# Kernel optimization log

Measured on AMD Instinct MI355X. Metric: run time of the kernel, lower is better.

Reference implementation:

```python
import jax, jax.numpy as jnp
import numpy as np

T, B, E, H, V = 512, 64, 512, 1024, 256


def setup_inputs() -> dict:
    key = jax.random.key(0)
    ks = jax.random.split(key, 10)
    s = lambda k, shape, sc: jax.random.normal(k, shape, dtype=jnp.float32) * sc
    return {
        "ints": jax.random.randint(ks[0], (T, B), 0, V),
        "encodings": s(ks[1], (V, E), 1.0),
        "output0": s(ks[2], (H,), 1.0),
        "memory0": s(ks[3], (H,), 1.0),
        "W_ih": s(ks[4], (4 * H, E), 0.03),
        "W_hh": s(ks[5], (4 * H, H), 0.03),
        "b_ih": s(ks[6], (4 * H,), 0.03),
        "b_hh": s(ks[7], (4 * H,), 0.03),
        "W_dec": s(ks[8], (V, H), 0.03),
        "b_dec": jnp.zeros((V,), dtype=jnp.float32),
    }


def reference(ints, encodings, output0, memory0, W_ih, W_hh, b_ih, b_hh, W_dec, b_dec):
    t, b = ints.shape
    h = output0.shape[0]
    x = encodings[ints]                                   # [T,B,E] embedding gather
    h0 = jnp.broadcast_to(output0, (b, h))                # learned initial hidden
    c0 = jnp.broadcast_to(memory0, (b, h))                # learned initial cell
    # precompute input projection for all timesteps (one big GEMM)
    x_proj = jnp.einsum('tbe,ge->tbg', x, W_ih) + b_ih + b_hh  # [T,B,4H]

    def step(carry, xp):
        hh, cc = carry
        gates = xp + hh @ W_hh.T                          # [B,4H]
        i, f, g, o = jnp.split(gates, 4, axis=-1)         # torch gate order i,f,g,o
        i = jax.nn.sigmoid(i)
        f = jax.nn.sigmoid(f)
        g = jnp.tanh(g)
        o = jax.nn.sigmoid(o)
        cc = f * cc + i * g
        hh = o * jnp.tanh(cc)
        return (hh, cc), hh

    _, hs = jax.lax.scan(step, (h0, c0), x_proj)          # [T,B,H]
    # outputs shifted right by one: predict char t from state after chars <t
    outs = jnp.concatenate([h0[None], hs[:-1]], axis=0)   # [T,B,H]
    return outs @ W_dec.T + b_dec                          # [T,B,V]
```

## Files before the change

### kernel.cpp

```cpp
#include <hip/hip_runtime.h>


#define TT 512
#define BB 64
#define HH 1024
#define VV 256
#define EE 512

typedef __attribute__((ext_vector_type(8))) short bf16x8;
typedef __attribute__((ext_vector_type(4))) float f32x4;
typedef __attribute__((ext_vector_type(4))) int i32x4;
typedef __attribute__((ext_vector_type(4))) unsigned short u16x4;

static __device__ __forceinline__ unsigned short f2bf(float f) {
  union { float f; unsigned u; } x; x.f = f;
  unsigned r = x.u + 0x7fffu + ((x.u >> 16) & 1u);
  return (unsigned short)(r >> 16);
}

__global__ void cvt_bf16(const float* __restrict__ s, unsigned short* __restrict__ d, int n4) {
  int i = blockIdx.x * blockDim.x + threadIdx.x;
  int st = gridDim.x * blockDim.x;
  for (; i < n4; i += st) {
    f32x4 v = *(const f32x4*)(s + 4l * i);
    u16x4 o;
    o.x = f2bf(v.x); o.y = f2bf(v.y); o.z = f2bf(v.z); o.w = f2bf(v.w);
    *(u16x4*)(d + 4l * i) = o;
  }
}

__global__ __launch_bounds__(256) void proj_kernel(
    const unsigned short* __restrict__ A,
    const unsigned short* __restrict__ Wi,
    const float* __restrict__ bih, const float* __restrict__ bhh,
    float* __restrict__ proj)
{
  __shared__ __align__(16) unsigned char Asm[64 * 128];
  const int tid = threadIdx.x;
  const int w = tid >> 6;
  const int lane = tid & 63;
  const int ln = lane & 15, kg = lane >> 4;
  const int m0 = blockIdx.x * 64;
  const int nb = blockIdx.y * 256 + w * 64;
  const int srow = tid >> 2, skq = tid & 3;

  f32x4 acc[4][4];
  for (int a = 0; a < 4; ++a) for (int b = 0; b < 4; ++b) acc[a][b] = (f32x4){0.f,0.f,0.f,0.f};

  for (int kc = 0; kc < 8; ++kc) {
    {
      const unsigned short* src = A + (m0 + srow) * 512 + kc * 64 + skq * 16;
      unsigned base = (unsigned)(srow * 128 + skq * 32);
      unsigned sw = (unsigned)((srow & 7) << 4);
      *(i32x4*)(Asm + ((base) ^ sw))      = *(const i32x4*)(src);
      *(i32x4*)(Asm + ((base + 16) ^ sw)) = *(const i32x4*)(src + 8);
    }
    __syncthreads();
    for (int kk = 0; kk < 2; ++kk) {
      bf16x8 afr[4];
      for (int mi = 0; mi < 4; ++mi) {
        int row = mi * 16 + ln;
        unsigned off = (unsigned)(row * 128 + (kk * 32 + kg * 8) * 2);
        afr[mi] = *(const bf16x8*)(Asm + (off ^ ((unsigned)(row & 7) << 4)));
      }
      for (int ni = 0; ni < 4; ++ni) {
        const unsigned short* bp = Wi + (nb + ni * 16 + ln) * 512 + kc * 64 + kk * 32 + kg * 8;
        bf16x8 bfr = *(const bf16x8*)bp;
        for (int mi = 0; mi < 4; ++mi)
          acc[mi][ni] = __builtin_amdgcn_mfma_f32_16x16x32_bf16(afr[mi], bfr, acc[mi][ni], 0, 0, 0);
      }
    }
    __syncthreads();
  }
  for (int ni = 0; ni < 4; ++ni) {
    int nn = nb + ni * 16 + ln;
    float bias = bih[nn] + bhh[nn];
    for (int mi = 0; mi < 4; ++mi) {
      int mr = m0 + mi * 16 + kg * 4;
      for (int r = 0; r < 4; ++r)
        proj[(mr + r) * 4096 + nn] = acc[mi][ni][r] + bias;
    }
  }
}

#define SPIN_CAP (1 << 16)

__global__ __launch_bounds__(256, 1) void scan_kernel(
    const unsigned short* __restrict__ Whh,
    const float* __restrict__ proj,
    const int* __restrict__ ints,
    const float* __restrict__ h0v,
    const float* __restrict__ c0v,
    unsigned short* __restrict__ outs,
    unsigned int* __restrict__ flags)
{
  __shared__ float gatesm[4][4][16][16];

  const int tid = threadIdx.x;
  const int blk = blockIdx.x;
  const int g = blk >> 6, j = blk & 63;
  const int w = tid >> 6, lane = tid & 63;
  const int ln = lane & 15, kg = lane >> 4;
  const int b = tid >> 4, u = tid & 15;
  const int uglob = j * 16 + u;
  const int bglob = g * 16 + b;

  bf16x8 bw[4][8];
#pragma unroll
  for (int gi = 0; gi < 4; ++gi)
#pragma unroll
    for (int kt = 0; kt < 8; ++kt)
      bw[gi][kt] = *(const bf16x8*)(Whh + (size_t)(gi * 1024 + j * 16 + ln) * 1024
                                        + w * 256 + kt * 32 + kg * 8);

  float c = c0v[uglob];

  {
    unsigned hb = f2bf(h0v[uglob]);
    unsigned short* op = outs + (size_t)bglob * 1024 + uglob;
    asm volatile("global_store_short %0, %1, off sc0 sc1" :: "v"(op), "v"(hb) : "memory");
    asm volatile("s_waitcnt vmcnt(0)" ::: "memory");
    if (lane == 0)
      __hip_atomic_store(&flags[(g * 4 + w) * 64 + j], 1u,
                         __ATOMIC_RELAXED, __HIP_MEMORY_SCOPE_AGENT);
  }

  const unsigned int* fb = flags + g * 256;

  for (int t = 0; t < TT - 1; ++t) {
    int vocab = ints[t * 64 + bglob];
    const float* pp = proj + (size_t)vocab * 4096 + uglob;
    float pr0 = pp[0];
    float pr1 = pp[1024];
    float pr2 = pp[2048];
    float pr3 = pp[3072];

    {
      unsigned tgt = (unsigned)(t + 1);
      int guard = 0;
      while (true) {
        unsigned f0 = __hip_atomic_load(fb +       lane, __ATOMIC_RELAXED, __HIP_MEMORY_SCOPE_AGENT);
        unsigned f1 = __hip_atomic_load(fb +  64 + lane, __ATOMIC_RELAXED, __HIP_MEMORY_SCOPE_AGENT);
        unsigned f2 = __hip_atomic_load(fb + 128 + lane, __ATOMIC_RELAXED, __HIP_MEMORY_SCOPE_AGENT);
        unsigned f3 = __hip_atomic_load(fb + 192 + lane, __ATOMIC_RELAXED, __HIP_MEMORY_SCOPE_AGENT);
        unsigned m0 = f0 < f1 ? f0 : f1;
        unsigned m1 = f2 < f3 ? f2 : f3;
        unsigned mm = m0 < m1 ? m0 : m1;
        if (__all((int)(mm >= tgt))) break;
        if (++guard > SPIN_CAP) break;
      }
    }
    asm volatile("" ::: "memory");

    i32x4 a[8];
    const unsigned short* ab = outs + (size_t)(t * 64 + g * 16 + ln) * 1024
                                    + w * 256 + kg * 8;
#define LOADA(i, off_lit) \
    asm volatile("global_load_dwordx4 %0, %1, off offset:" off_lit " sc0 sc1" \
                 : "=v"(a[i]) : "v"(ab) : "memory")
    LOADA(0, "0");   LOADA(1, "64");  LOADA(2, "128"); LOADA(3, "192");
    LOADA(4, "256"); LOADA(5, "320"); LOADA(6, "384"); LOADA(7, "448");
#undef LOADA
    asm volatile("s_waitcnt vmcnt(0)" ::: "memory");
    __builtin_amdgcn_sched_barrier(0);

    f32x4 ac0 = (f32x4){0.f,0.f,0.f,0.f}, ac1 = ac0, ac2 = ac0, ac3 = ac0;
#pragma unroll
    for (int kt = 0; kt < 8; ++kt) {
      union { i32x4 i; bf16x8 h; } av; av.i = a[kt];
      ac0 = __builtin_amdgcn_mfma_f32_16x16x32_bf16(av.h, bw[0][kt], ac0, 0, 0, 0);
      ac1 = __builtin_amdgcn_mfma_f32_16x16x32_bf16(av.h, bw[1][kt], ac1, 0, 0, 0);
      ac2 = __builtin_amdgcn_mfma_f32_16x16x32_bf16(av.h, bw[2][kt], ac2, 0, 0, 0);
      ac3 = __builtin_amdgcn_mfma_f32_16x16x32_bf16(av.h, bw[3][kt], ac3, 0, 0, 0);
    }

#pragma unroll
    for (int r = 0; r < 4; ++r) {
      gatesm[w][0][kg * 4 + r][ln] = ac0[r];
      gatesm[w][1][kg * 4 + r][ln] = ac1[r];
      gatesm[w][2][kg * 4 + r][ln] = ac2[r];
      gatesm[w][3][kg * 4 + r][ln] = ac3[r];
    }
    __syncthreads();

    float gi_ = pr0, gf_ = pr1, gg_ = pr2, go_ = pr3;
#pragma unroll
    for (int ww = 0; ww < 4; ++ww) {
      gi_ += gatesm[ww][0][b][u];
      gf_ += gatesm[ww][1][b][u];
      gg_ += gatesm[ww][2][b][u];
      go_ += gatesm[ww][3][b][u];
    }
    float ii = __builtin_amdgcn_rcpf(1.f + __expf(-gi_));
    float ff = __builtin_amdgcn_rcpf(1.f + __expf(-gf_));
    float gt = 1.f - 2.f * __builtin_amdgcn_rcpf(1.f + __expf(2.f * gg_));
    float oo = __builtin_amdgcn_rcpf(1.f + __expf(-go_));
    c = ff * c + ii * gt;
    float hv = oo * (1.f - 2.f * __builtin_amdgcn_rcpf(1.f + __expf(2.f * c)));

    {
      unsigned hb = f2bf(hv);
      unsigned short* op = outs + (size_t)((t + 1) * 64 + bglob) * 1024 + uglob;
      asm volatile("global_store_short %0, %1, off sc0 sc1" :: "v"(op), "v"(hb) : "memory");
      asm volatile("s_waitcnt vmcnt(0)" ::: "memory");
      if (lane == 0)
        __hip_atomic_store(&flags[(g * 4 + w) * 64 + j], (unsigned)(t + 2),
                           __ATOMIC_RELAXED, __HIP_MEMORY_SCOPE_AGENT);
    }
  }
}

__global__ __launch_bounds__(256) void decode_kernel(
    const unsigned short* __restrict__ A,
    const unsigned short* __restrict__ Wd,
    const float* __restrict__ bdec,
    float* __restrict__ out)
{
  __shared__ __align__(16) unsigned char Asm[64 * 128];
  const int tid = threadIdx.x;
  const int w = tid >> 6;
  const int lane = tid & 63;
  const int ln = lane & 15, kg = lane >> 4;
  const int m0 = blockIdx.x * 64;
  const int nb = w * 64;
  const int srow = tid >> 2, skq = tid & 3;

  f32x4 acc[4][4];
  for (int a = 0; a < 4; ++a) for (int b = 0; b < 4; ++b) acc[a][b] = (f32x4){0.f,0.f,0.f,0.f};

  for (int kc = 0; kc < 16; ++kc) {
    {
      const unsigned short* src = A + (m0 + srow) * 1024 + kc * 64 + skq * 16;
      unsigned base = (unsigned)(srow * 128 + skq * 32);
      unsigned sw = (unsigned)((srow & 7) << 4);
      *(i32x4*)(Asm + ((base) ^ sw))      = *(const i32x4*)(src);
      *(i32x4*)(Asm + ((base + 16) ^ sw)) = *(const i32x4*)(src + 8);
    }
    __syncthreads();
    for (int kk = 0; kk < 2; ++kk) {
      bf16x8 afr[4];
      for (int mi = 0; mi < 4; ++mi) {
        int row = mi * 16 + ln;
        unsigned off = (unsigned)(row * 128 + (kk * 32 + kg * 8) * 2);
        afr[mi] = *(const bf16x8*)(Asm + (off ^ ((unsigned)(row & 7) << 4)));
      }
      for (int ni = 0; ni < 4; ++ni) {
        const unsigned short* bp = Wd + (nb + ni * 16 + ln) * 1024 + kc * 64 + kk * 32 + kg * 8;
        bf16x8 bfr = *(const bf16x8*)bp;
        for (int mi = 0; mi < 4; ++mi)
          acc[mi][ni] = __builtin_amdgcn_mfma_f32_16x16x32_bf16(afr[mi], bfr, acc[mi][ni], 0, 0, 0);
      }
    }
    __syncthreads();
  }
  for (int ni = 0; ni < 4; ++ni) {
    int nn = nb + ni * 16 + ln;
    float bd = bdec[nn];
    for (int mi = 0; mi < 4; ++mi) {
      int mr = m0 + mi * 16 + kg * 4;
      for (int r = 0; r < 4; ++r)
        out[(mr + r) * 256 + nn] = acc[mi][ni][r] + bd;
    }
  }
}

extern "C" void kernel_launch(void* const* d_in, const int* in_sizes, int n_in,
                              void* d_out, int out_size, void* d_ws, size_t ws_size,
                              hipStream_t stream) {
  const int*   ints = (const int*)  d_in[0];
  const float* enc  = (const float*)d_in[1];
  const float* out0 = (const float*)d_in[2];
  const float* mem0 = (const float*)d_in[3];
  const float* Wih  = (const float*)d_in[4];
  const float* Whh  = (const float*)d_in[5];
  const float* bih  = (const float*)d_in[6];
  const float* bhh  = (const float*)d_in[7];
  const float* Wdec = (const float*)d_in[8];
  const float* bdec = (const float*)d_in[9];
  float* out = (float*)d_out;

  char* ws = (char*)d_ws;
  size_t off = 0;
  auto alloc = [&](size_t bytes) { char* p = ws + off; off += (bytes + 255) & ~(size_t)255; return p; };
  unsigned short* Whh_bf  = (unsigned short*)alloc(4096ull * 1024 * 2);
  unsigned short* enc_bf  = (unsigned short*)alloc(256ull * 512 * 2);
  unsigned short* Wih_bf  = (unsigned short*)alloc(4096ull * 512 * 2);
  unsigned short* Wdec_bf = (unsigned short*)alloc(256ull * 1024 * 2);
  float*          proj    = (float*)alloc(256ull * 4096 * 4);
  unsigned short* outs_bf = (unsigned short*)alloc(512ull * 64 * 1024 * 2);
  unsigned int*   flags   = (unsigned int*)alloc(1024 * 4);

  hipMemsetAsync(flags, 0, 1024 * 4, stream);

  cvt_bf16<<<512, 256, 0, stream>>>(Whh,  Whh_bf,  4096 * 1024 / 4);
  cvt_bf16<<<64,  256, 0, stream>>>(enc,  enc_bf,  256 * 512 / 4);
  cvt_bf16<<<256, 256, 0, stream>>>(Wih,  Wih_bf,  4096 * 512 / 4);
  cvt_bf16<<<64,  256, 0, stream>>>(Wdec, Wdec_bf, 256 * 1024 / 4);

  proj_kernel<<<dim3(4, 16), 256, 0, stream>>>(enc_bf, Wih_bf, bih, bhh, proj);

  {
    const unsigned short* a0 = Whh_bf;
    const float* a1 = proj;
    const int* a2 = ints;
    const float* a3 = out0;
    const float* a4 = mem0;
    unsigned short* a5 = outs_bf;
    unsigned int* a6 = flags;
    void* args[] = { &a0, &a1, &a2, &a3, &a4, &a5, &a6 };
    hipError_t e = hipLaunchCooperativeKernel((const void*)scan_kernel,
                                              dim3(256), dim3(256), args, 0, stream);
    if (e != hipSuccess) {
      scan_kernel<<<256, 256, 0, stream>>>(Whh_bf, proj, ints, out0, mem0,
                                           outs_bf, flags);
    }
  }

  decode_kernel<<<512, 256, 0, stream>>>(outs_bf, Wdec_bf, bdec, out);
}
```

Before: 1.910 ms.

## Replace flag-based step barrier with sequence-tagged hidden-state words in double buffer

```diff
diff --git a/kernel.cpp b/kernel.cpp
--- a/kernel.cpp
+++ b/kernel.cpp
@@ -83,7 +83,7 @@
   }
 }
 
-#define SPIN_CAP (1 << 16)
+#define SPIN_CAP 16384
 
 __global__ __launch_bounds__(256, 1) void scan_kernel(
     const unsigned short* __restrict__ Whh,
@@ -91,8 +91,8 @@
     const int* __restrict__ ints,
     const float* __restrict__ h0v,
     const float* __restrict__ c0v,
-    unsigned short* __restrict__ outs,
-    unsigned int* __restrict__ flags)
+    unsigned int* __restrict__ hcomm,
+    unsigned short* __restrict__ outs)
 {
   __shared__ float gatesm[4][4][16][16];
 
@@ -116,16 +116,13 @@
   float c = c0v[uglob];
 
   {
-    unsigned hb = f2bf(h0v[uglob]);
-    unsigned short* op = outs + (size_t)bglob * 1024 + uglob;
-    asm volatile("global_store_short %0, %1, off sc0 sc1" :: "v"(op), "v"(hb) : "memory");
-    asm volatile("s_waitcnt vmcnt(0)" ::: "memory");
-    if (lane == 0)
-      __hip_atomic_store(&flags[(g * 4 + w) * 64 + j], 1u,
-                         __ATOMIC_RELAXED, __HIP_MEMORY_SCOPE_AGENT);
-  }
-
-  const unsigned int* fb = flags + g * 256;
+    float hv0 = h0v[uglob];
+    unsigned short hb = f2bf(hv0);
+    unsigned word = ((unsigned)hb << 16) | 1u;
+    unsigned* hp = hcomm + 65536 + (size_t)bglob * 1024 + uglob;
+    asm volatile("global_store_dword %0, %1, off sc0 sc1" :: "v"(hp), "v"(word) : "memory");
+    outs[(size_t)bglob * 1024 + uglob] = hb;
+  }
 
   for (int t = 0; t < TT - 1; ++t) {
     int vocab = ints[t * 64 + bglob];
@@ -135,43 +132,57 @@
     float pr2 = pp[2048];
     float pr3 = pp[3072];
 
+    const unsigned* ab = hcomm + ((size_t)((t + 1) & 1)) * 65536
+                       + (size_t)(g * 16 + ln) * 1024 + w * 256 + kg * 8;
+    unsigned tgt = (unsigned)(t + 1);
+    i32x4 q[16];
     {
-      unsigned tgt = (unsigned)(t + 1);
       int guard = 0;
       while (true) {
-        unsigned f0 = __hip_atomic_load(fb +       lane, __ATOMIC_RELAXED, __HIP_MEMORY_SCOPE_AGENT);
-        unsigned f1 = __hip_atomic_load(fb +  64 + lane, __ATOMIC_RELAXED, __HIP_MEMORY_SCOPE_AGENT);
-        unsigned f2 = __hip_atomic_load(fb + 128 + lane, __ATOMIC_RELAXED, __HIP_MEMORY_SCOPE_AGENT);
-        unsigned f3 = __hip_atomic_load(fb + 192 + lane, __ATOMIC_RELAXED, __HIP_MEMORY_SCOPE_AGENT);
-        unsigned m0 = f0 < f1 ? f0 : f1;
-        unsigned m1 = f2 < f3 ? f2 : f3;
-        unsigned mm = m0 < m1 ? m0 : m1;
-        if (__all((int)(mm >= tgt))) break;
+#define LQ(i, off_lit) \
+        asm volatile("global_load_dwordx4 %0, %1, off offset:" off_lit " sc0 sc1" \
+                     : "=v"(q[i]) : "v"(ab) : "memory")
+        LQ(0, "0");    LQ(1, "16");   LQ(2, "128");  LQ(3, "144");
+        LQ(4, "256");  LQ(5, "272");  LQ(6, "384");  LQ(7, "400");
+        LQ(8, "512");  LQ(9, "528");  LQ(10, "640"); LQ(11, "656");
+        LQ(12, "768"); LQ(13, "784"); LQ(14, "896"); LQ(15, "912");
+#undef LQ
+        asm volatile("s_waitcnt vmcnt(0)" ::: "memory");
+        __builtin_amdgcn_sched_barrier(0);
+        unsigned bad = 0;
+#pragma unroll
+        for (int i = 0; i < 16; ++i) {
+          bad |= ((unsigned)q[i].x ^ tgt);
+          bad |= ((unsigned)q[i].y ^ tgt);
+          bad |= ((unsigned)q[i].z ^ tgt);
+          bad |= ((unsigned)q[i].w ^ tgt);
+        }
+        if (__all((bad & 0xffffu) == 0u)) break;
         if (++guard > SPIN_CAP) break;
       }
     }
-    asm volatile("" ::: "memory");
-
-    i32x4 a[8];
-    const unsigned short* ab = outs + (size_t)(t * 64 + g * 16 + ln) * 1024
-                                    + w * 256 + kg * 8;
-#define LOADA(i, off_lit) \
-    asm volatile("global_load_dwordx4 %0, %1, off offset:" off_lit " sc0 sc1" \
-                 : "=v"(a[i]) : "v"(ab) : "memory")
-    LOADA(0, "0");   LOADA(1, "64");  LOADA(2, "128"); LOADA(3, "192");
-    LOADA(4, "256"); LOADA(5, "320"); LOADA(6, "384"); LOADA(7, "448");
-#undef LOADA
-    asm volatile("s_waitcnt vmcnt(0)" ::: "memory");
     __builtin_amdgcn_sched_barrier(0);
 
+    bf16x8 av[8];
+#pragma unroll
+    for (int kt = 0; kt < 8; ++kt) {
+      i32x4 lo = q[2 * kt], hi = q[2 * kt + 1];
+      unsigned d0 = ((unsigned)lo.x >> 16) | ((unsigned)lo.y & 0xffff0000u);
+      unsigned d1 = ((unsigned)lo.z >> 16) | ((unsigned)lo.w & 0xffff0000u);
+      unsigned d2 = ((unsigned)hi.x >> 16) | ((unsigned)hi.y & 0xffff0000u);
+      unsigned d3 = ((unsigned)hi.z >> 16) | ((unsigned)hi.w & 0xffff0000u);
+      union { i32x4 i; bf16x8 h; } u2;
+      u2.i = (i32x4){ (int)d0, (int)d1, (int)d2, (int)d3 };
+      av[kt] = u2.h;
+    }
+
     f32x4 ac0 = (f32x4){0.f,0.f,0.f,0.f}, ac1 = ac0, ac2 = ac0, ac3 = ac0;
 #pragma unroll
     for (int kt = 0; kt < 8; ++kt) {
-      union { i32x4 i; bf16x8 h; } av; av.i = a[kt];
-      ac0 = __builtin_amdgcn_mfma_f32_16x16x32_bf16(av.h, bw[0][kt], ac0, 0, 0, 0);
-      ac1 = __builtin_amdgcn_mfma_f32_16x16x32_bf16(av.h, bw[1][kt], ac1, 0, 0, 0);
-      ac2 = __builtin_amdgcn_mfma_f32_16x16x32_bf16(av.h, bw[2][kt], ac2, 0, 0, 0);
-      ac3 = __builtin_amdgcn_mfma_f32_16x16x32_bf16(av.h, bw[3][kt], ac3, 0, 0, 0);
+      ac0 = __builtin_amdgcn_mfma_f32_16x16x32_bf16(av[kt], bw[0][kt], ac0, 0, 0, 0);
+      ac1 = __builtin_amdgcn_mfma_f32_16x16x32_bf16(av[kt], bw[1][kt], ac1, 0, 0, 0);
+      ac2 = __builtin_amdgcn_mfma_f32_16x16x32_bf16(av[kt], bw[2][kt], ac2, 0, 0, 0);
+      ac3 = __builtin_amdgcn_mfma_f32_16x16x32_bf16(av[kt], bw[3][kt], ac3, 0, 0, 0);
     }
 
 #pragma unroll
@@ -199,14 +210,14 @@
     float hv = oo * (1.f - 2.f * __builtin_amdgcn_rcpf(1.f + __expf(2.f * c)));
 
     {
-      unsigned hb = f2bf(hv);
-      unsigned short* op = outs + (size_t)((t + 1) * 64 + bglob) * 1024 + uglob;
-      asm volatile("global_store_short %0, %1, off sc0 sc1" :: "v"(op), "v"(hb) : "memory");
-      asm volatile("s_waitcnt vmcnt(0)" ::: "memory");
-      if (lane == 0)
-        __hip_atomic_store(&flags[(g * 4 + w) * 64 + j], (unsigned)(t + 2),
-                           __ATOMIC_RELAXED, __HIP_MEMORY_SCOPE_AGENT);
-    }
+      unsigned short hb = f2bf(hv);
+      unsigned word = ((unsigned)hb << 16) | ((unsigned)(t + 2) & 0xffffu);
+      unsigned* hp = hcomm + ((size_t)((t + 2) & 1)) * 65536
+                   + (size_t)bglob * 1024 + uglob;
+      asm volatile("global_store_dword %0, %1, off sc0 sc1" :: "v"(hp), "v"(word) : "memory");
+      outs[(size_t)(t + 1) * 65536 + (size_t)bglob * 1024 + uglob] = hb;
+    }
+    __syncthreads();
   }
 }
 
@@ -288,9 +299,9 @@
   unsigned short* Wdec_bf = (unsigned short*)alloc(256ull * 1024 * 2);
   float*          proj    = (float*)alloc(256ull * 4096 * 4);
   unsigned short* outs_bf = (unsigned short*)alloc(512ull * 64 * 1024 * 2);
-  unsigned int*   flags   = (unsigned int*)alloc(1024 * 4);
-
-  hipMemsetAsync(flags, 0, 1024 * 4, stream);
+  unsigned int*   hcomm   = (unsigned int*)alloc(2ull * 64 * 1024 * 4);
+
+  hipMemsetAsync(hcomm, 0, 2ull * 64 * 1024 * 4, stream);
 
   cvt_bf16<<<512, 256, 0, stream>>>(Whh,  Whh_bf,  4096 * 1024 / 4);
   cvt_bf16<<<64,  256, 0, stream>>>(enc,  enc_bf,  256 * 512 / 4);
@@ -305,14 +316,14 @@
     const int* a2 = ints;
     const float* a3 = out0;
     const float* a4 = mem0;
-    unsigned short* a5 = outs_bf;
-    unsigned int* a6 = flags;
+    unsigned int* a5 = hcomm;
+    unsigned short* a6 = outs_bf;
     void* args[] = { &a0, &a1, &a2, &a3, &a4, &a5, &a6 };
     hipError_t e = hipLaunchCooperativeKernel((const void*)scan_kernel,
                                               dim3(256), dim3(256), args, 0, stream);
     if (e != hipSuccess) {
       scan_kernel<<<256, 256, 0, stream>>>(Whh_bf, proj, ints, out0, mem0,
-                                           outs_bf, flags);
+                                           hcomm, outs_bf);
     }
   }
 
```

Result: slower. 2.156 ms (+12.9%).
